# Performance work log

Measured on AMD Instinct MI355X. Metric: run time of the kernel, lower is better.

Reference implementation:

```python
import jax, jax.numpy as jnp
import numpy as np

H = 128   # hidden_size
DYN = 2   # dynamic_features


def setup_inputs() -> dict:
    B, S, STAT = 256, 64, 2
    key = jax.random.key(0)
    ks = jax.random.split(key, 9)
    sc = 0.05
    return {
        "static": jax.random.normal(ks[0], (B, STAT, S), jnp.float32),
        "static_embeddings": jax.random.normal(ks[1], (B, H, S), jnp.float32),
        "dynamic": jax.random.uniform(ks[2], (B, DYN, S), jnp.float32),
        # dynamic_embedding: Conv1d(2 -> 128, k=1)
        "dyn_w": jax.random.normal(ks[3], (H, DYN), jnp.float32) * sc,
        "dyn_b": jnp.zeros((H,), jnp.float32),
        # decoder_input_dynamic_embedding: Conv1d(128 -> 128, k=1)
        "in_w": jax.random.normal(ks[4], (H, H), jnp.float32) * sc,
        "in_b": jnp.zeros((H,), jnp.float32),
        # GRU (single layer, batch_first), torch gate order r,z,n
        "w_ih": jax.random.normal(ks[5], (3 * H, H), jnp.float32) * sc,
        "w_hh": jax.random.normal(ks[6], (3 * H, H), jnp.float32) * sc,
        "b_ih": jnp.zeros((3 * H,), jnp.float32),
        "b_hh": jnp.zeros((3 * H,), jnp.float32),
        # DoubleAttention: scores = v . tanh(W [static; dynamic; hidden])
        "W_att": jax.random.normal(ks[7], (H, 3 * H), jnp.float32) * sc,
        "v_att": jax.random.normal(ks[8], (H,), jnp.float32) * sc,
    }


def _pointer_forward(static_embeddings, dynamic, dyn_w, dyn_b, in_w, in_b,
                     w_ih, w_hh, b_ih, b_hh, W_att, v_att):
    B, Hd, S = static_embeddings.shape
    NEG = jnp.asarray(-1e9, static_embeddings.dtype)
    base = jax.random.key(42)

    def gru_cell(x, h):  # torch nn.GRU single step
        gi = x @ w_ih.T + b_ih
        gh = h @ w_hh.T + b_hh
        ir, iz, i_n = jnp.split(gi, 3, axis=-1)
        hr, hz, h_n = jnp.split(gh, 3, axis=-1)
        r = jax.nn.sigmoid(ir + hr)
        z = jax.nn.sigmoid(iz + hz)
        n = jnp.tanh(i_n + r * h_n)
        return (1.0 - z) * n + z * h

    first_mask = jnp.zeros((B, S), static_embeddings.dtype).at[:, 0].set(1.0)

    def step(carry, i):
        dec_in, h, visited, dyn = carry
        # decoder_input_dynamic_embedding: 1x1 conv == per-token linear
        x = dec_in @ in_w.T + in_b                      # [B,H]
        h = gru_cell(x, h)                              # decoder_output == new hidden
        # i==0: only depot (index 0) is selectable; afterwards: unvisited nodes
        mask = jnp.where(i == 0, first_mask, 1.0 - visited)
        dyn_emb = jnp.einsum('bds,hd->bhs', dyn, dyn_w) + dyn_b[None, :, None]
        ctx = jnp.concatenate(
            [static_embeddings, dyn_emb,
             jnp.broadcast_to(h[:, :, None], (B, Hd, S))], axis=1)  # [B,3H,S]
        scores = jnp.einsum('h,bhs->bs', v_att,
                            jnp.tanh(jnp.einsum('hk,bks->bhs', W_att, ctx)))
        logits = jnp.where(mask > 0, scores, NEG)       # -inf on masked positions
        ptr = jax.random.categorical(jax.random.fold_in(base, i), logits)  # sample
        logp = jnp.take_along_axis(jax.nn.log_softmax(logits, -1),
                                   ptr[:, None], axis=1)[:, 0]
        sel = (jnp.arange(S)[None, :] == ptr[:, None]).astype(dyn.dtype)  # [B,S]
        visited = jnp.maximum(visited, sel)
        dyn = dyn * (1.0 - sel)[:, None, :]             # update_dynamic_state
        # original feeds the (conv-transformed) decoder input back to itself
        return (x, h, visited, dyn), (ptr, logp)

    init = (static_embeddings[:, :, 0],                  # decoder_input = emb of node 0
            jnp.zeros((B, Hd), static_embeddings.dtype),  # GRU hidden
            jnp.zeros((B, S), static_embeddings.dtype),   # visited
            dynamic)
    _, (tours, logps) = jax.lax.scan(step, init, jnp.arange(S))
    return tours.T, logps.T  # [B,S], [B,S]


def reference(static, static_embeddings, dynamic, dyn_w, dyn_b, in_w, in_b,
              w_ih, w_hh, b_ih, b_hh, W_att, v_att):
    # dropout layers are identity in eval mode; `static` is only used for logging
    return _pointer_forward(static_embeddings, dynamic, dyn_w, dyn_b, in_w, in_b,
                            w_ih, w_hh, b_ih, b_hh, W_att, v_att)
```

## Files before the change

kernel.cpp:

```cpp
#include <hip/hip_runtime.h>
#include <stdint.h>


#define BN 256
#define SN 64
#define HN 128
#define NEGV (-1.0e9f)
#define TINYF 1.17549435e-38f

#define OFF_A   0
#define OFF_GI  8192
#define OFF_WHC 8192
#define OFF_SET 16384
#define OFF_UT  24832
#define OFF_HC  33280
#define OFF_KK  33536
#define OFF_SV  33664
#define OFF_DY  33792
#define OFF_WD  33920
#define OFF_CV  34176
#define SMEM_FLOATS 34304

typedef float v4f __attribute__((ext_vector_type(4)));

struct W8 { v4f a, b, c, d, e, f, g, h; };
struct W4 { v4f a, b, c, d; };

__device__ __forceinline__ W8 ldg8_s64(const float* p) {
  W8 r;
  asm volatile(
      "global_load_dwordx4 %0, %8, off\n\t"
      "global_load_dwordx4 %1, %8, off offset:64\n\t"
      "global_load_dwordx4 %2, %8, off offset:128\n\t"
      "global_load_dwordx4 %3, %8, off offset:192\n\t"
      "global_load_dwordx4 %4, %8, off offset:256\n\t"
      "global_load_dwordx4 %5, %8, off offset:320\n\t"
      "global_load_dwordx4 %6, %8, off offset:384\n\t"
      "global_load_dwordx4 %7, %8, off offset:448\n\t"
      "s_waitcnt vmcnt(0)"
      : "=&v"(r.a), "=&v"(r.b), "=&v"(r.c), "=&v"(r.d),
        "=&v"(r.e), "=&v"(r.f), "=&v"(r.g), "=&v"(r.h)
      : "v"(p));
  return r;
}

__device__ __forceinline__ W4 ldg4_s128(const float* p) {
  W4 r;
  asm volatile(
      "global_load_dwordx4 %0, %4, off\n\t"
      "global_load_dwordx4 %1, %4, off offset:128\n\t"
      "global_load_dwordx4 %2, %4, off offset:256\n\t"
      "global_load_dwordx4 %3, %4, off offset:384\n\t"
      "s_waitcnt vmcnt(0)"
      : "=&v"(r.a), "=&v"(r.b), "=&v"(r.c), "=&v"(r.d)
      : "v"(p));
  return r;
}

__device__ __forceinline__ float dot8(const W8& w, const float4* x4) {
  float a0 = 0.f, a1 = 0.f, a2 = 0.f, a3 = 0.f;
  a0 = fmaf(w.a.x, x4[0].x, a0); a1 = fmaf(w.a.y, x4[0].y, a1);
  a2 = fmaf(w.a.z, x4[0].z, a2); a3 = fmaf(w.a.w, x4[0].w, a3);
  a0 = fmaf(w.b.x, x4[1].x, a0); a1 = fmaf(w.b.y, x4[1].y, a1);
  a2 = fmaf(w.b.z, x4[1].z, a2); a3 = fmaf(w.b.w, x4[1].w, a3);
  a0 = fmaf(w.c.x, x4[2].x, a0); a1 = fmaf(w.c.y, x4[2].y, a1);
  a2 = fmaf(w.c.z, x4[2].z, a2); a3 = fmaf(w.c.w, x4[2].w, a3);
  a0 = fmaf(w.d.x, x4[3].x, a0); a1 = fmaf(w.d.y, x4[3].y, a1);
  a2 = fmaf(w.d.z, x4[3].z, a2); a3 = fmaf(w.d.w, x4[3].w, a3);
  a0 = fmaf(w.e.x, x4[4].x, a0); a1 = fmaf(w.e.y, x4[4].y, a1);
  a2 = fmaf(w.e.z, x4[4].z, a2); a3 = fmaf(w.e.w, x4[4].w, a3);
  a0 = fmaf(w.f.x, x4[5].x, a0); a1 = fmaf(w.f.y, x4[5].y, a1);
  a2 = fmaf(w.f.z, x4[5].z, a2); a3 = fmaf(w.f.w, x4[5].w, a3);
  a0 = fmaf(w.g.x, x4[6].x, a0); a1 = fmaf(w.g.y, x4[6].y, a1);
  a2 = fmaf(w.g.z, x4[6].z, a2); a3 = fmaf(w.g.w, x4[6].w, a3);
  a0 = fmaf(w.h.x, x4[7].x, a0); a1 = fmaf(w.h.y, x4[7].y, a1);
  a2 = fmaf(w.h.z, x4[7].z, a2); a3 = fmaf(w.h.w, x4[7].w, a3);
  return (a0 + a1) + (a2 + a3);
}

__device__ __forceinline__ void dot4x2(const W4& w0, const W4& w1,
                                       const float4* x4, float& s0o, float& s1o) {
  float a00 = 0.f, a01 = 0.f, a10 = 0.f, a11 = 0.f;
  a00 = fmaf(w0.a.x, x4[0].x, a00); a01 = fmaf(w0.a.y, x4[0].y, a01);
  a00 = fmaf(w0.a.z, x4[0].z, a00); a01 = fmaf(w0.a.w, x4[0].w, a01);
  a10 = fmaf(w1.a.x, x4[0].x, a10); a11 = fmaf(w1.a.y, x4[0].y, a11);
  a10 = fmaf(w1.a.z, x4[0].z, a10); a11 = fmaf(w1.a.w, x4[0].w, a11);
  a00 = fmaf(w0.b.x, x4[1].x, a00); a01 = fmaf(w0.b.y, x4[1].y, a01);
  a00 = fmaf(w0.b.z, x4[1].z, a00); a01 = fmaf(w0.b.w, x4[1].w, a01);
  a10 = fmaf(w1.b.x, x4[1].x, a10); a11 = fmaf(w1.b.y, x4[1].y, a11);
  a10 = fmaf(w1.b.z, x4[1].z, a10); a11 = fmaf(w1.b.w, x4[1].w, a11);
  a00 = fmaf(w0.c.x, x4[2].x, a00); a01 = fmaf(w0.c.y, x4[2].y, a01);
  a00 = fmaf(w0.c.z, x4[2].z, a00); a01 = fmaf(w0.c.w, x4[2].w, a01);
  a10 = fmaf(w1.c.x, x4[2].x, a10); a11 = fmaf(w1.c.y, x4[2].y, a11);
  a10 = fmaf(w1.c.z, x4[2].z, a10); a11 = fmaf(w1.c.w, x4[2].w, a11);
  a00 = fmaf(w0.d.x, x4[3].x, a00); a01 = fmaf(w0.d.y, x4[3].y, a01);
  a00 = fmaf(w0.d.z, x4[3].z, a00); a01 = fmaf(w0.d.w, x4[3].w, a01);
  a10 = fmaf(w1.d.x, x4[3].x, a10); a11 = fmaf(w1.d.y, x4[3].y, a11);
  a10 = fmaf(w1.d.z, x4[3].z, a10); a11 = fmaf(w1.d.w, x4[3].w, a11);
  s0o = a00 + a01; s1o = a10 + a11;
}

__device__ __forceinline__ uint32_t rotl32(uint32_t v, int d) {
  return (v << d) | (v >> (32 - d));
}

__device__ __forceinline__ void threefry2x32(uint32_t k0, uint32_t k1,
                                             uint32_t x0, uint32_t x1,
                                             uint32_t& o0, uint32_t& o1) {
  uint32_t ks2 = k0 ^ k1 ^ 0x1BD11BDAu;
  x0 += k0; x1 += k1;
  x0 += x1; x1 = rotl32(x1, 13); x1 ^= x0;
  x0 += x1; x1 = rotl32(x1, 15); x1 ^= x0;
  x0 += x1; x1 = rotl32(x1, 26); x1 ^= x0;
  x0 += x1; x1 = rotl32(x1, 6);  x1 ^= x0;
  x0 += k1; x1 += ks2 + 1u;
  x0 += x1; x1 = rotl32(x1, 17); x1 ^= x0;
  x0 += x1; x1 = rotl32(x1, 29); x1 ^= x0;
  x0 += x1; x1 = rotl32(x1, 16); x1 ^= x0;
  x0 += x1; x1 = rotl32(x1, 24); x1 ^= x0;
  x0 += ks2; x1 += k0 + 2u;
  x0 += x1; x1 = rotl32(x1, 13); x1 ^= x0;
  x0 += x1; x1 = rotl32(x1, 15); x1 ^= x0;
  x0 += x1; x1 = rotl32(x1, 26); x1 ^= x0;
  x0 += x1; x1 = rotl32(x1, 6);  x1 ^= x0;
  x0 += k0; x1 += k1 + 3u;
  x0 += x1; x1 = rotl32(x1, 17); x1 ^= x0;
  x0 += x1; x1 = rotl32(x1, 29); x1 ^= x0;
  x0 += x1; x1 = rotl32(x1, 16); x1 ^= x0;
  x0 += x1; x1 = rotl32(x1, 24); x1 ^= x0;
  x0 += k1; x1 += ks2 + 4u;
  x0 += x1; x1 = rotl32(x1, 13); x1 ^= x0;
  x0 += x1; x1 = rotl32(x1, 15); x1 ^= x0;
  x0 += x1; x1 = rotl32(x1, 26); x1 ^= x0;
  x0 += x1; x1 = rotl32(x1, 6);  x1 ^= x0;
  x0 += ks2; x1 += k0 + 5u;
  o0 = x0; o1 = x1;
}

__device__ __forceinline__ float jax_gumbel(uint32_t k0, uint32_t k1, int j) {
  uint32_t o0, o1;
  threefry2x32(k0, k1, 0u, (uint32_t)j, o0, o1);
  uint32_t bits = o0 ^ o1;
  uint32_t ub = (bits >> 9) | 0x3F800000u;
  float u = __uint_as_float(ub) - 1.0f;
  u = fmaxf(u + TINYF, TINYF);
  return -logf(-logf(u));
}

__device__ __forceinline__ float ftanh(float x) {
  float ax = fabsf(x);
  float e = __expf(-2.0f * ax);
  float r = (1.0f - e) * __builtin_amdgcn_rcpf(1.0f + e);
  return copysignf(r, x);
}

__device__ __forceinline__ float fsig(float x) {
  return __builtin_amdgcn_rcpf(1.0f + __expf(-x));
}

__global__ void k0_dyn(const float* __restrict__ W_att, const float* __restrict__ dyn_w,
                       const float* __restrict__ dyn_b, float* __restrict__ Wd,
                       float* __restrict__ cv) {
  int h = threadIdx.x;
  float w0 = 0.f, w1 = 0.f, cc = 0.f;
  for (int k = 0; k < HN; ++k) {
    float w = W_att[h * 384 + 128 + k];
    w0 = fmaf(w, dyn_w[2 * k + 0], w0);
    w1 = fmaf(w, dyn_w[2 * k + 1], w1);
    cc = fmaf(w, dyn_b[k], cc);
  }
  Wd[2 * h] = w0; Wd[2 * h + 1] = w1; cv[h] = cc;
}

__global__ __launch_bounds__(512, 2)
void mega(
    const float* __restrict__ SE, const float* __restrict__ dynamic,
    const float* __restrict__ in_w, const float* __restrict__ in_b,
    const float* __restrict__ w_ih, const float* __restrict__ b_ih,
    const float* __restrict__ w_hh, const float* __restrict__ b_hh,
    const float* __restrict__ W_att, const float* __restrict__ v_att,
    const float* __restrict__ Wd, const float* __restrict__ cv,
    float* __restrict__ out) {
  extern __shared__ float sm[];
  int b = blockIdx.x, t = threadIdx.x;
  float* A   = sm + OFF_A;
  float* GIl = sm + OFF_GI;
  float* WHC = sm + OFF_WHC;
  float* SET = sm + OFF_SET;
  float* UT  = sm + OFF_UT;
  float* HC  = sm + OFF_HC;
  uint32_t* KK = (uint32_t*)(sm + OFF_KK);
  float* SV  = sm + OFF_SV;
  float* DY  = sm + OFF_DY;
  float* WDs = sm + OFF_WD;
  float* CVs = sm + OFF_CV;

  if (t < 64) {
    uint32_t o0, o1;
    threefry2x32(0u, 42u, 0u, (uint32_t)t, o0, o1);
    KK[2 * t] = o0; KK[2 * t + 1] = o1;
  }
  if (t < 128) {
    SV[t]  = v_att[t];
    DY[t]  = dynamic[b * 128 + t];
    CVs[t] = cv[t];
    HC[t]  = SE[b * 8192 + t * 64];
  }
  if (t < 256) WDs[t] = Wd[t];
  __syncthreads();

  {
    int ml = t >> 2, ks = t & 3;
    W8 wv = ldg8_s64(in_w + ml * HN + ks * 4);
    float bib = in_b[ml];
    for (int ii = 0; ii < SN; ++ii) {
      const float* xc = HC + (ii & 1) * 128;
      float* xn = HC + ((ii + 1) & 1) * 128;
      float4 x4[8];
#pragma unroll
      for (int q = 0; q < 8; ++q)
        x4[q] = *(const float4*)(xc + q * 16 + ks * 4);
      float s = dot8(wv, x4);
      s += __shfl_xor(s, 1); s += __shfl_xor(s, 2);
      if (ks == 0) {
        float xv = s + bib;
        A[ii * 128 + ml] = xv;
        xn[ml] = xv;
      }
      __syncthreads();
    }
  }

  {
    int ml = t >> 2, ks = t & 3;
    W8 wv0 = ldg8_s64(w_ih + (ml)       * HN + ks * 4);
    W8 wv1 = ldg8_s64(w_ih + (ml + 128) * HN + ks * 4);
    W8 wv2 = ldg8_s64(w_ih + (ml + 256) * HN + ks * 4);
    float bi0 = b_ih[ml], bi1 = b_ih[ml + 128], bi2 = b_ih[ml + 256];
    for (int n = 0; n < SN; ++n) {
      float4 x4[8];
#pragma unroll
      for (int q = 0; q < 8; ++q)
        x4[q] = *(const float4*)(A + n * 128 + q * 16 + ks * 4);
      float s0 = dot8(wv0, x4);
      float s1 = dot8(wv1, x4);
      float s2 = dot8(wv2, x4);
      s0 += __shfl_xor(s0, 1); s0 += __shfl_xor(s0, 2);
      s1 += __shfl_xor(s1, 1); s1 += __shfl_xor(s1, 2);
      s2 += __shfl_xor(s2, 1); s2 += __shfl_xor(s2, 2);
      if (ks == 0) {
        GIl[n * 384 + ml]       = s0 + bi0;
        GIl[n * 384 + ml + 128] = s1 + bi1;
        GIl[n * 384 + ml + 256] = s2 + bi2;
      }
    }
    __syncthreads();
  }

  if (t < 256) HC[t] = 0.f;
  __syncthreads();
  {
    int ml = t >> 2, ks = t & 3;
    W8 wv0 = ldg8_s64(w_hh + (ml)       * HN + ks * 4);
    W8 wv1 = ldg8_s64(w_hh + (ml + 128) * HN + ks * 4);
    W8 wv2 = ldg8_s64(w_hh + (ml + 256) * HN + ks * 4);
    float bh0 = b_hh[ml], bh1 = b_hh[ml + 128], bh2 = b_hh[ml + 256];
    float hp = 0.f;
    for (int ii = 0; ii < SN; ++ii) {
      const float* hcr = HC + (ii & 1) * 128;
      float* hcw = HC + ((ii + 1) & 1) * 128;
      float4 x4[8];
#pragma unroll
      for (int q = 0; q < 8; ++q)
        x4[q] = *(const float4*)(hcr + q * 16 + ks * 4);
      float s0 = dot8(wv0, x4);
      float s1 = dot8(wv1, x4);
      float s2 = dot8(wv2, x4);
      s0 += __shfl_xor(s0, 1); s0 += __shfl_xor(s0, 2);
      s1 += __shfl_xor(s1, 1); s1 += __shfl_xor(s1, 2);
      s2 += __shfl_xor(s2, 1); s2 += __shfl_xor(s2, 2);
      if (ks == 0) {
        const float* gr = GIl + ii * 384;
        float r = fsig(gr[ml] + s0 + bh0);
        float z = fsig(gr[128 + ml] + s1 + bh1);
        float nn = ftanh(gr[256 + ml] + r * (s2 + bh2));
        float hn = (1.0f - z) * nn + z * hp;
        hcw[ml] = hn;
        A[ii * 128 + ml] = hn;
        hp = hn;
      }
      __syncthreads();
    }
  }

  {
    int ml = t >> 3, ks = t & 7;
    W4 w0 = ldg4_s128(W_att + (ml)      * 384 + 256 + ks * 4);
    W4 w1 = ldg4_s128(W_att + (ml + 64) * 384 + 256 + ks * 4);
    for (int n = 0; n < SN; ++n) {
      float4 x4[4];
#pragma unroll
      for (int q = 0; q < 4; ++q)
        x4[q] = *(const float4*)(A + n * 128 + q * 32 + ks * 4);
      float s0, s1;
      dot4x2(w0, w1, x4, s0, s1);
      s0 += __shfl_xor(s0, 1); s0 += __shfl_xor(s0, 2); s0 += __shfl_xor(s0, 4);
      s1 += __shfl_xor(s1, 1); s1 += __shfl_xor(s1, 2); s1 += __shfl_xor(s1, 4);
      if (ks == 0) { WHC[n * 128 + ml] = s0; WHC[n * 128 + ml + 64] = s1; }
    }
    __syncthreads();
  }

  for (int p = 0; p < 16; ++p) {
    int idx = p * 512 + t;
    int h = idx >> 6, s = idx & 63;
    SET[s * 132 + h] = SE[b * 8192 + idx];
  }
  __syncthreads();

  {
    int ml = t >> 3, ks = t & 7;
    W4 w0 = ldg4_s128(W_att + (ml)      * 384 + ks * 4);
    W4 w1 = ldg4_s128(W_att + (ml + 64) * 384 + ks * 4);
    for (int n = 0; n < SN; ++n) {
      float4 x4[4];
#pragma unroll
      for (int q = 0; q < 4; ++q)
        x4[q] = *(const float4*)(SET + n * 132 + q * 32 + ks * 4);
      float s0, s1;
      dot4x2(w0, w1, x4, s0, s1);
      s0 += __shfl_xor(s0, 1); s0 += __shfl_xor(s0, 2); s0 += __shfl_xor(s0, 4);
      s1 += __shfl_xor(s1, 1); s1 += __shfl_xor(s1, 2); s1 += __shfl_xor(s1, 4);
      if (ks == 0) {
        float d0 = DY[n], d1 = DY[64 + n];
        UT[(ml)      * 66 + n] = s0 + WDs[2 * ml] * d0 + WDs[2 * ml + 1] * d1 + CVs[ml];
        UT[(ml + 64) * 66 + n] = s1 + WDs[2 * (ml + 64)] * d0 + WDs[2 * (ml + 64) + 1] * d1 + CVs[ml + 64];
      }
    }
    __syncthreads();
  }

  {
    int s = t & 63, w = t >> 6;
    float acc[8];
#pragma unroll
    for (int j = 0; j < 8; ++j) acc[j] = 0.f;
    for (int h = 0; h < HN; h += 4) {
      float u0 = UT[(h + 0) * 66 + s];
      float u1 = UT[(h + 1) * 66 + s];
      float u2 = UT[(h + 2) * 66 + s];
      float u3 = UT[(h + 3) * 66 + s];
      float4 v4 = *(const float4*)(SV + h);
#pragma unroll
      for (int j = 0; j < 8; ++j) {
        float4 wh = *(const float4*)(WHC + (w * 8 + j) * 128 + h);
        float a = acc[j];
        a = fmaf(v4.x, ftanh(u0 + wh.x), a);
        a = fmaf(v4.y, ftanh(u1 + wh.y), a);
        a = fmaf(v4.z, ftanh(u2 + wh.z), a);
        a = fmaf(v4.w, ftanh(u3 + wh.w), a);
        acc[j] = a;
      }
    }
    __syncthreads();
#pragma unroll
    for (int j = 0; j < 8; ++j) A[(w * 8 + j) * 64 + s] = acc[j];
    __syncthreads();
  }

  {
    float* G = A + 4096;
    for (int p = 0; p < 8; ++p) {
      int idx = p * 512 + t;
      int i = idx >> 6;
      G[idx] = jax_gumbel(KK[2 * i], KK[2 * i + 1], b * 64 + (idx & 63));
    }
    __syncthreads();
  }

  if (t < 64) {
    const float* Pl = A;
    const float* Gl = A + 4096;
    int s = t;
    bool visited = false;
    for (int i = 0; i < SN; ++i) {
      float score = Pl[i * 64 + s];
      bool allowed = (i == 0) ? (s == 0) : (!visited);
      float logit = allowed ? score : NEGV;
      float z = logit + Gl[i * 64 + s];
      float bz = z; int bi = s;
#pragma unroll
      for (int off = 32; off > 0; off >>= 1) {
        float oz = __shfl_xor(bz, off);
        int oi = __shfl_xor(bi, off);
        if (oz > bz || (oz == bz && oi < bi)) { bz = oz; bi = oi; }
      }
      int ptr = bi;
      float m = logit;
#pragma unroll
      for (int off = 32; off > 0; off >>= 1) m = fmaxf(m, __shfl_xor(m, off));
      float e = expf(logit - m);
      float sum = e;
#pragma unroll
      for (int off = 32; off > 0; off >>= 1) sum += __shfl_xor(sum, off);
      float chosen = __shfl(logit, ptr);
      float logp = (chosen - m) - logf(sum);
      if (s == ptr) visited = true;
      if (s == 0) {
        out[b * SN + i] = (float)ptr;
        out[BN * SN + b * SN + i] = logp;
      }
    }
  }
}

extern "C" void kernel_launch(void* const* d_in, const int* in_sizes, int n_in,
                              void* d_out, int out_size, void* d_ws, size_t ws_size,
                              hipStream_t stream) {
  const float* SE    = (const float*)d_in[1];
  const float* dynam = (const float*)d_in[2];
  const float* dyn_w = (const float*)d_in[3];
  const float* dyn_b = (const float*)d_in[4];
  const float* in_w  = (const float*)d_in[5];
  const float* in_b  = (const float*)d_in[6];
  const float* w_ih  = (const float*)d_in[7];
  const float* w_hh  = (const float*)d_in[8];
  const float* b_ih2 = (const float*)d_in[9];
  const float* b_hh  = (const float*)d_in[10];
  const float* W_att = (const float*)d_in[11];
  const float* v_att = (const float*)d_in[12];
  float* out = (float*)d_out;
  float* ws = (float*)d_ws;

  float* Wd = ws;
  float* cv = ws + 256;

  (void)hipFuncSetAttribute((const void*)mega,
                            hipFuncAttributeMaxDynamicSharedMemorySize,
                            SMEM_FLOATS * 4);

  hipLaunchKernelGGL(k0_dyn, dim3(1), dim3(128), 0, stream,
                     W_att, dyn_w, dyn_b, Wd, cv);
  hipLaunchKernelGGL(mega, dim3(BN), dim3(512), SMEM_FLOATS * 4, stream,
                     SE, dynam, in_w, in_b, w_ih, b_ih2, w_hh, b_hh,
                     W_att, v_att, Wd, cv, out);
}
```

Measured before the change: 322.2 us.

## Retile batched projections as register-blocked GEMMs with 16 tokens per thread

Restructures the three non-recurrent projections (input-gate GRU projection, hidden-to-attention, and static-embedding-to-attention) so that each thread owns one output row and accumulates 16 tokens in registers. Weights are streamed from global memory in float4 chunks instead of being held in registers with cross-lane shuffle reductions. This removes the per-token shuffle reductions and the idle lanes that only write when ks==0, and reuses each weight load across 16 tokens. In exchange it raises register pressure from the 48 accumulators, repeatedly loads weights from global or cache, and its LDS reads are broadcast-style. Occupancy is also re-specified through the amdgpu_waves_per_eu attribute.

```diff
diff --git a/kernel.cpp b/kernel.cpp
--- a/kernel.cpp
+++ b/kernel.cpp
@@ -24,7 +24,6 @@
 typedef float v4f __attribute__((ext_vector_type(4)));
 
 struct W8 { v4f a, b, c, d, e, f, g, h; };
-struct W4 { v4f a, b, c, d; };
 
 __device__ __forceinline__ W8 ldg8_s64(const float* p) {
   W8 r;
@@ -40,19 +39,6 @@
       "s_waitcnt vmcnt(0)"
       : "=&v"(r.a), "=&v"(r.b), "=&v"(r.c), "=&v"(r.d),
         "=&v"(r.e), "=&v"(r.f), "=&v"(r.g), "=&v"(r.h)
-      : "v"(p));
-  return r;
-}
-
-__device__ __forceinline__ W4 ldg4_s128(const float* p) {
-  W4 r;
-  asm volatile(
-      "global_load_dwordx4 %0, %4, off\n\t"
-      "global_load_dwordx4 %1, %4, off offset:128\n\t"
-      "global_load_dwordx4 %2, %4, off offset:256\n\t"
-      "global_load_dwordx4 %3, %4, off offset:384\n\t"
-      "s_waitcnt vmcnt(0)"
-      : "=&v"(r.a), "=&v"(r.b), "=&v"(r.c), "=&v"(r.d)
       : "v"(p));
   return r;
 }
@@ -76,28 +62,6 @@
   a0 = fmaf(w.h.x, x4[7].x, a0); a1 = fmaf(w.h.y, x4[7].y, a1);
   a2 = fmaf(w.h.z, x4[7].z, a2); a3 = fmaf(w.h.w, x4[7].w, a3);
   return (a0 + a1) + (a2 + a3);
-}
-
-__device__ __forceinline__ void dot4x2(const W4& w0, const W4& w1,
-                                       const float4* x4, float& s0o, float& s1o) {
-  float a00 = 0.f, a01 = 0.f, a10 = 0.f, a11 = 0.f;
-  a00 = fmaf(w0.a.x, x4[0].x, a00); a01 = fmaf(w0.a.y, x4[0].y, a01);
-  a00 = fmaf(w0.a.z, x4[0].z, a00); a01 = fmaf(w0.a.w, x4[0].w, a01);
-  a10 = fmaf(w1.a.x, x4[0].x, a10); a11 = fmaf(w1.a.y, x4[0].y, a11);
-  a10 = fmaf(w1.a.z, x4[0].z, a10); a11 = fmaf(w1.a.w, x4[0].w, a11);
-  a00 = fmaf(w0.b.x, x4[1].x, a00); a01 = fmaf(w0.b.y, x4[1].y, a01);
-  a00 = fmaf(w0.b.z, x4[1].z, a00); a01 = fmaf(w0.b.w, x4[1].w, a01);
-  a10 = fmaf(w1.b.x, x4[1].x, a10); a11 = fmaf(w1.b.y, x4[1].y, a11);
-  a10 = fmaf(w1.b.z, x4[1].z, a10); a11 = fmaf(w1.b.w, x4[1].w, a11);
-  a00 = fmaf(w0.c.x, x4[2].x, a00); a01 = fmaf(w0.c.y, x4[2].y, a01);
-  a00 = fmaf(w0.c.z, x4[2].z, a00); a01 = fmaf(w0.c.w, x4[2].w, a01);
-  a10 = fmaf(w1.c.x, x4[2].x, a10); a11 = fmaf(w1.c.y, x4[2].y, a11);
-  a10 = fmaf(w1.c.z, x4[2].z, a10); a11 = fmaf(w1.c.w, x4[2].w, a11);
-  a00 = fmaf(w0.d.x, x4[3].x, a00); a01 = fmaf(w0.d.y, x4[3].y, a01);
-  a00 = fmaf(w0.d.z, x4[3].z, a00); a01 = fmaf(w0.d.w, x4[3].w, a01);
-  a10 = fmaf(w1.d.x, x4[3].x, a10); a11 = fmaf(w1.d.y, x4[3].y, a11);
-  a10 = fmaf(w1.d.z, x4[3].z, a10); a11 = fmaf(w1.d.w, x4[3].w, a11);
-  s0o = a00 + a01; s1o = a10 + a11;
 }
 
 __device__ __forceinline__ uint32_t rotl32(uint32_t v, int d) {
@@ -172,7 +136,8 @@
   Wd[2 * h] = w0; Wd[2 * h + 1] = w1; cv[h] = cc;
 }
 
-__global__ __launch_bounds__(512, 2)
+__global__ __launch_bounds__(512)
+__attribute__((amdgpu_waves_per_eu(2, 2)))
 void mega(
     const float* __restrict__ SE, const float* __restrict__ dynamic,
     const float* __restrict__ in_w, const float* __restrict__ in_b,
@@ -232,27 +197,45 @@
   }
 
   {
-    int ml = t >> 2, ks = t & 3;
-    W8 wv0 = ldg8_s64(w_ih + (ml)       * HN + ks * 4);
-    W8 wv1 = ldg8_s64(w_ih + (ml + 128) * HN + ks * 4);
-    W8 wv2 = ldg8_s64(w_ih + (ml + 256) * HN + ks * 4);
-    float bi0 = b_ih[ml], bi1 = b_ih[ml + 128], bi2 = b_ih[ml + 256];
-    for (int n = 0; n < SN; ++n) {
-      float4 x4[8];
-#pragma unroll
-      for (int q = 0; q < 8; ++q)
-        x4[q] = *(const float4*)(A + n * 128 + q * 16 + ks * 4);
-      float s0 = dot8(wv0, x4);
-      float s1 = dot8(wv1, x4);
-      float s2 = dot8(wv2, x4);
-      s0 += __shfl_xor(s0, 1); s0 += __shfl_xor(s0, 2);
-      s1 += __shfl_xor(s1, 1); s1 += __shfl_xor(s1, 2);
-      s2 += __shfl_xor(s2, 1); s2 += __shfl_xor(s2, 2);
-      if (ks == 0) {
-        GIl[n * 384 + ml]       = s0 + bi0;
-        GIl[n * 384 + ml + 128] = s1 + bi1;
-        GIl[n * 384 + ml + 256] = s2 + bi2;
-      }
+    int r = t & 127, cg = t >> 7;
+    const float* xb = A + cg * 16 * 128;
+    const float* w0p = w_ih + (r)       * HN;
+    const float* w1p = w_ih + (r + 128) * HN;
+    const float* w2p = w_ih + (r + 256) * HN;
+    float acc[3][16];
+#pragma unroll
+    for (int g = 0; g < 3; ++g)
+#pragma unroll
+      for (int i = 0; i < 16; ++i) acc[g][i] = 0.f;
+#pragma unroll 1
+    for (int k = 0; k < HN; k += 4) {
+      float4 w0 = *(const float4*)(w0p + k);
+      float4 w1 = *(const float4*)(w1p + k);
+      float4 w2 = *(const float4*)(w2p + k);
+#pragma unroll
+      for (int i = 0; i < 16; ++i) {
+        float4 xv = *(const float4*)(xb + i * 128 + k);
+        acc[0][i] = fmaf(w0.x, xv.x, acc[0][i]);
+        acc[0][i] = fmaf(w0.y, xv.y, acc[0][i]);
+        acc[0][i] = fmaf(w0.z, xv.z, acc[0][i]);
+        acc[0][i] = fmaf(w0.w, xv.w, acc[0][i]);
+        acc[1][i] = fmaf(w1.x, xv.x, acc[1][i]);
+        acc[1][i] = fmaf(w1.y, xv.y, acc[1][i]);
+        acc[1][i] = fmaf(w1.z, xv.z, acc[1][i]);
+        acc[1][i] = fmaf(w1.w, xv.w, acc[1][i]);
+        acc[2][i] = fmaf(w2.x, xv.x, acc[2][i]);
+        acc[2][i] = fmaf(w2.y, xv.y, acc[2][i]);
+        acc[2][i] = fmaf(w2.z, xv.z, acc[2][i]);
+        acc[2][i] = fmaf(w2.w, xv.w, acc[2][i]);
+      }
+    }
+    float b0 = b_ih[r], b1 = b_ih[r + 128], b2 = b_ih[r + 256];
+#pragma unroll
+    for (int i = 0; i < 16; ++i) {
+      int n = cg * 16 + i;
+      GIl[n * 384 + r]       = acc[0][i] + b0;
+      GIl[n * 384 + 128 + r] = acc[1][i] + b1;
+      GIl[n * 384 + 256 + r] = acc[2][i] + b2;
     }
     __syncthreads();
   }
@@ -294,20 +277,27 @@
   }
 
   {
-    int ml = t >> 3, ks = t & 7;
-    W4 w0 = ldg4_s128(W_att + (ml)      * 384 + 256 + ks * 4);
-    W4 w1 = ldg4_s128(W_att + (ml + 64) * 384 + 256 + ks * 4);
-    for (int n = 0; n < SN; ++n) {
-      float4 x4[4];
-#pragma unroll
-      for (int q = 0; q < 4; ++q)
-        x4[q] = *(const float4*)(A + n * 128 + q * 32 + ks * 4);
-      float s0, s1;
-      dot4x2(w0, w1, x4, s0, s1);
-      s0 += __shfl_xor(s0, 1); s0 += __shfl_xor(s0, 2); s0 += __shfl_xor(s0, 4);
-      s1 += __shfl_xor(s1, 1); s1 += __shfl_xor(s1, 2); s1 += __shfl_xor(s1, 4);
-      if (ks == 0) { WHC[n * 128 + ml] = s0; WHC[n * 128 + ml + 64] = s1; }
-    }
+    int r = t & 127, cg = t >> 7;
+    const float* xb = A + cg * 16 * 128;
+    const float* wp = W_att + r * 384 + 256;
+    float acc[16];
+#pragma unroll
+    for (int i = 0; i < 16; ++i) acc[i] = 0.f;
+#pragma unroll 1
+    for (int k = 0; k < HN; k += 4) {
+      float4 w = *(const float4*)(wp + k);
+#pragma unroll
+      for (int i = 0; i < 16; ++i) {
+        float4 xv = *(const float4*)(xb + i * 128 + k);
+        acc[i] = fmaf(w.x, xv.x, acc[i]);
+        acc[i] = fmaf(w.y, xv.y, acc[i]);
+        acc[i] = fmaf(w.z, xv.z, acc[i]);
+        acc[i] = fmaf(w.w, xv.w, acc[i]);
+      }
+    }
+#pragma unroll
+    for (int i = 0; i < 16; ++i)
+      WHC[(cg * 16 + i) * 128 + r] = acc[i];
     __syncthreads();
   }
 
@@ -319,23 +309,29 @@
   __syncthreads();
 
   {
-    int ml = t >> 3, ks = t & 7;
-    W4 w0 = ldg4_s128(W_att + (ml)      * 384 + ks * 4);
-    W4 w1 = ldg4_s128(W_att + (ml + 64) * 384 + ks * 4);
-    for (int n = 0; n < SN; ++n) {
-      float4 x4[4];
-#pragma unroll
-      for (int q = 0; q < 4; ++q)
-        x4[q] = *(const float4*)(SET + n * 132 + q * 32 + ks * 4);
-      float s0, s1;
-      dot4x2(w0, w1, x4, s0, s1);
-      s0 += __shfl_xor(s0, 1); s0 += __shfl_xor(s0, 2); s0 += __shfl_xor(s0, 4);
-      s1 += __shfl_xor(s1, 1); s1 += __shfl_xor(s1, 2); s1 += __shfl_xor(s1, 4);
-      if (ks == 0) {
-        float d0 = DY[n], d1 = DY[64 + n];
-        UT[(ml)      * 66 + n] = s0 + WDs[2 * ml] * d0 + WDs[2 * ml + 1] * d1 + CVs[ml];
-        UT[(ml + 64) * 66 + n] = s1 + WDs[2 * (ml + 64)] * d0 + WDs[2 * (ml + 64) + 1] * d1 + CVs[ml + 64];
-      }
+    int r = t & 127, cg = t >> 7;
+    const float* xb = SET + cg * 16 * 132;
+    const float* wp = W_att + r * 384;
+    float acc[16];
+#pragma unroll
+    for (int i = 0; i < 16; ++i) acc[i] = 0.f;
+#pragma unroll 1
+    for (int k = 0; k < HN; k += 4) {
+      float4 w = *(const float4*)(wp + k);
+#pragma unroll
+      for (int i = 0; i < 16; ++i) {
+        float4 xv = *(const float4*)(xb + i * 132 + k);
+        acc[i] = fmaf(w.x, xv.x, acc[i]);
+        acc[i] = fmaf(w.y, xv.y, acc[i]);
+        acc[i] = fmaf(w.z, xv.z, acc[i]);
+        acc[i] = fmaf(w.w, xv.w, acc[i]);
+      }
+    }
+    float wd0 = WDs[2 * r], wd1 = WDs[2 * r + 1], cvv = CVs[r];
+#pragma unroll
+    for (int i = 0; i < 16; ++i) {
+      int n = cg * 16 + i;
+      UT[r * 66 + n] = acc[i] + wd0 * DY[n] + wd1 * DY[64 + n] + cvv;
     }
     __syncthreads();
   }
```

New measurement: 317.8 us. Within noise of the previous version (-1.4%).
